# Kernel optimization log

Hardware: AMD Instinct MI355X
Metric: run time of the kernel (lower is better)

Reference implementation:

```python
import jax, jax.numpy as jnp
import numpy as np

B, H, W, C = 2, 96, 192, 768
NH, HD = 12, 64
W0, W1 = 8, 8          # window size
S0, S1 = 4, 4          # shift size
N = W0 * W1
NW = (H // W0) * (W // W1)
HID = 3072             # mlp_ratio 4 * dim
SCALE = HD ** -0.5


def _ln(x, g, b):
    m = x.mean(-1, keepdims=True)
    v = ((x - m) ** 2).mean(-1, keepdims=True)
    return (x - m) * jax.lax.rsqrt(v + 1e-5) * g + b


def _partition(x):  # (B,H,W,C) -> (B*NW, W0, W1, C)
    Bb = x.shape[0]
    x = x.reshape(Bb, H // W0, W0, W // W1, W1, -1).transpose(0, 1, 3, 2, 4, 5)
    return x.reshape(-1, W0, W1, x.shape[-1])


def _reverse(w):  # (B*NW, W0, W1, C) -> (B,H,W,C)
    Cc = w.shape[-1]
    x = w.reshape(B, H // W0, W // W1, W0, W1, Cc).transpose(0, 1, 3, 2, 4, 5)
    return x.reshape(B, H, W, Cc)


def _rope2(x):  # axial 2D RoPE on (nB, W0, W1, HD): first half rotates over h, second over w
    dh = HD // 2

    def cs(L, d):
        inv = 1.0 / (10000.0 ** (jnp.arange(0, d, 2, dtype=jnp.float32) / d))
        ang = jnp.arange(L, dtype=jnp.float32)[:, None] * inv
        return jnp.cos(ang), jnp.sin(ang)

    def rot(xa, cos, sin):
        x1, x2 = xa[..., 0::2], xa[..., 1::2]
        return jnp.stack([x1 * cos - x2 * sin, x1 * sin + x2 * cos], -1).reshape(xa.shape)

    ch, sh = cs(W0, dh)
    cw, sw = cs(W1, dh)
    xh = rot(x[..., :dh], ch[:, None, :], sh[:, None, :])
    xw = rot(x[..., dh:], cw[None, :, :], sw[None, :, :])
    return jnp.concatenate([xh, xw], -1)


def _make_mask():
    # faithful port of BasicLayer.create_mask (2D path)
    img = np.zeros((H, W), np.float32)
    cnt = 0
    for hs in (slice(0, -W0), slice(-W0, -S0), slice(-S0, None)):
        for wsl in (slice(0, -W1), slice(-W1, 0), slice(0, None)):
            img[hs, wsl] = cnt
            cnt += 1
    mw = img.reshape(H // W0, W0, W // W1, W1).transpose(0, 2, 1, 3).reshape(NW, N)
    am = mw[:, None, :] - mw[:, :, None]
    return jnp.asarray(np.where(am != 0, -100.0, 0.0).astype(np.float32))


def setup_inputs():
    key = jax.random.key(0)
    ks = jax.random.split(key, 6)
    s = lambda k, shape, fan: jax.random.normal(k, shape, jnp.float32) * (fan ** -0.5)
    return dict(
        x=jax.random.normal(ks[0], (B, H * W, C), jnp.float32),
        mask=_make_mask(),
        w_qkv=s(ks[1], (3 * C, C), C), b_qkv=jnp.zeros((3 * C,), jnp.float32),
        w_proj=s(ks[2], (C, C), C), b_proj=jnp.zeros((C,), jnp.float32),
        g1=jnp.ones((C,), jnp.float32), b1=jnp.zeros((C,), jnp.float32),
        g2=jnp.ones((C,), jnp.float32), b2=jnp.zeros((C,), jnp.float32),
        w_fc1=s(ks[3], (HID, C), C), b_fc1=jnp.zeros((HID,), jnp.float32),
        w_fc2=s(ks[4], (C, HID), HID), b_fc2=jnp.zeros((C,), jnp.float32),
    )


def reference(x, mask, w_qkv, b_qkv, w_proj, b_proj, g1, b1, g2, b2,
              w_fc1, b_fc1, w_fc2, b_fc2):
    shortcut = x
    xi = x.reshape(B, H, W, C)
    xi = jnp.roll(xi, (-S0, -S1), axis=(1, 2))
    xw = _partition(xi).reshape(-1, N, C)  # (B*NW, N, C)
    B_ = xw.shape[0]
    qkv = (xw @ w_qkv.T + b_qkv).reshape(B_, N, 3, NH, HD).transpose(2, 0, 3, 1, 4)
    q, k, v = qkv[0], qkv[1], qkv[2]  # (B_, NH, N, HD)
    q = _rope2(q.reshape(-1, W0, W1, HD)).reshape(B_, NH, N, HD)
    k = _rope2(k.reshape(-1, W0, W1, HD)).reshape(B_, NH, N, HD)
    attn = jnp.einsum('bhnd,bhmd->bhnm', q * SCALE, k)
    attn = attn.reshape(B, NW, NH, N, N) + mask[None, :, None]
    attn = jax.nn.softmax(attn.reshape(B_, NH, N, N), axis=-1)
    out = jnp.einsum('bhnm,bhmd->bnhd', attn, v).reshape(B_, N, C)
    out = out @ w_proj.T + b_proj
    xr = _reverse(out.reshape(-1, W0, W1, C))
    xr = jnp.roll(xr, (S0, S1), axis=(1, 2)).reshape(B, H * W, C)
    x1 = _ln(shortcut + xr, g1, b1)          # post-norm residual, as in source
    h = jax.nn.relu(x1 @ w_fc1.T + b_fc1) @ w_fc2.T + b_fc2
    return _ln(x1 + h, g2, b2)
```

## Files before the change

### kernel.cpp

```cpp
#include <hip/hip_runtime.h>
#include <math.h>
#include <stddef.h>

#define NTOK   36864
#define CDIM   768
#define HIDDIM 3072
#define QKVDIM 2304

typedef unsigned short u16;
typedef unsigned int   u32;
typedef __attribute__((ext_vector_type(8))) short short8;
typedef __attribute__((ext_vector_type(4))) float f32x4;

__device__ __forceinline__ float bf2f(u16 h) { return __uint_as_float(((u32)h) << 16); }
__device__ __forceinline__ u16 f2bf(float f) {
  u32 u = __float_as_uint(f);
  u32 r = u + 0x7fffu + ((u >> 16) & 1u);
  return (u16)(r >> 16);
}

__device__ __forceinline__ int win_row_to_src(int r) {
  int n = r & 63;
  int wflat = r >> 6;
  int b = wflat / 288;
  int wi = wflat - b * 288;
  int wh = wi / 24;
  int ww = wi - wh * 24;
  int i0 = n >> 3, i1 = n & 7;
  int hh = wh * 8 + i0 + 4; if (hh >= 96)  hh -= 96;
  int wp = ww * 8 + i1 + 4; if (wp >= 192) wp -= 192;
  return b * 18432 + hh * 192 + wp;
}

__device__ __forceinline__ void load_lds16(const u16* g, u16* l) {
  __builtin_amdgcn_global_load_lds((const __attribute__((address_space(1))) void*)g,
                                   (__attribute__((address_space(3))) void*)l, 16, 0, 0);
}

template<int OUTBF, int RELU, int RES>
__launch_bounds__(256)
__global__ void gemm_mfma(const u16* __restrict__ A, const u16* __restrict__ Wt,
                          const float* __restrict__ bias, const u16* __restrict__ res,
                          void* __restrict__ Cout, int M, int N, int K,
                          int gridx, int nwg)
{
  const int orig = blockIdx.x;
  const int xcd  = orig & 7;
  const int q    = nwg >> 3, r8 = nwg & 7;
  const int wgid = (xcd < r8 ? xcd * (q + 1) : r8 * (q + 1) + (xcd - r8) * q) + (orig >> 3);
  const int halfn = nwg >> 1, hc = gridx >> 1;
  const int half  = (wgid >= halfn) ? 1 : 0;
  const int w2    = wgid - half * halfn;
  const int bn    = (w2 % hc + half * hc) * 128;
  const int bm    = (w2 / hc) * 128;

  __shared__ u16 As[128 * 64];
  __shared__ u16 Bs[128 * 64];
  const int t    = threadIdx.x;
  const int wv   = t >> 6, lane = t & 63;
  const int wm   = wv >> 1, wn = wv & 1;
  const int lr   = lane & 15, lg = lane >> 4;
  const int srow = t >> 3;
  const int sslot= t & 7;

  const u16* Abase = A  + (size_t)bm * K;
  const u16* Bbase = Wt + (size_t)bn * K;

  f32x4 acc[4][4] = {};

  for (int k0 = 0; k0 < K; k0 += 64) {
#pragma unroll
    for (int i = 0; i < 4; i++) {
      int row  = i * 32 + srow;
      int slot = sslot ^ (row & 7);
      load_lds16(Abase + (size_t)row * K + k0 + slot * 8, As + t * 8 + i * 2048);
      load_lds16(Bbase + (size_t)row * K + k0 + slot * 8, Bs + t * 8 + i * 2048);
    }
    __syncthreads();

    short8 av[2][4], bv[2][4];
#pragma unroll
    for (int ks = 0; ks < 2; ks++) {
#pragma unroll
      for (int f = 0; f < 4; f++) {
        int ra = wm * 64 + f * 16 + lr;
        av[ks][f] = *(const short8*)(As + ra * 64 + (((ks * 4 + lg) ^ (ra & 7)) << 3));
        int rb = wn * 64 + f * 16 + lr;
        bv[ks][f] = *(const short8*)(Bs + rb * 64 + (((ks * 4 + lg) ^ (rb & 7)) << 3));
      }
    }
#pragma unroll
    for (int ks = 0; ks < 2; ks++)
#pragma unroll
      for (int mf = 0; mf < 4; mf++)
#pragma unroll
        for (int nf = 0; nf < 4; nf++)
          acc[mf][nf] = __builtin_amdgcn_mfma_f32_16x16x32_bf16(av[ks][mf], bv[ks][nf], acc[mf][nf], 0, 0, 0);
    __syncthreads();
  }

#pragma unroll
  for (int nf = 0; nf < 4; nf++) {
    int col = bn + wn * 64 + nf * 16 + lr;
    float bcol = bias[col];
#pragma unroll
    for (int mf = 0; mf < 4; mf++) {
#pragma unroll
      for (int j = 0; j < 4; j++) {
        int row = bm + wm * 64 + mf * 16 + lg * 4 + j;
        float v = acc[mf][nf][j] + bcol;
        if (RELU) v = fmaxf(v, 0.f);
        if (RES)  v += bf2f(res[(size_t)row * N + col]);
        if (OUTBF) ((u16*)Cout)[(size_t)row * N + col] = f2bf(v);
        else       ((float*)Cout)[(size_t)row * N + col] = v;
      }
    }
  }
}

__launch_bounds__(256)
__global__ void gather_x_bf16(const float* __restrict__ x, u16* __restrict__ xg)
{
  const int r = blockIdx.x, t = threadIdx.x;
  const float* src = x + (size_t)win_row_to_src(r) * CDIM;
  u16* dst = xg + (size_t)r * CDIM;
#pragma unroll
  for (int e = 0; e < 3; e++) dst[t + 256 * e] = f2bf(src[t + 256 * e]);
}

__launch_bounds__(256)
__global__ void conv_bf16(const float* __restrict__ in, u16* __restrict__ out, int n)
{
  int i = blockIdx.x * 256 + threadIdx.x;
  if (i < n) out[i] = f2bf(in[i]);
}

__launch_bounds__(256)
__global__ void attn_mfma(const u16* __restrict__ qkv, const float* __restrict__ mask,
                          u16* __restrict__ out, int bw0)
{
  __shared__ u16 vt[4][4096];
  __shared__ u16 pbuf[4][4096];
  __shared__ float ropetab[512];

  const int t = threadIdx.x;
  {
    int p = t >> 3, pos = t & 7;
    float inv = __expf(-(float)(p & 15) * 0.5756462732485115f);
    float sv, cv;
    sincosf((float)pos * inv, &sv, &cv);
    ropetab[t * 2]     = cv;
    ropetab[t * 2 + 1] = sv;
  }
  __syncthreads();

  const int wv = t >> 6, lane = t & 63;
  const int lr = lane & 15, lg = lane >> 4;
  const int gp   = blockIdx.x * 4 + wv;
  const int head = gp % 12;
  const int lw   = gp / 12;
  const int bwg  = bw0 + lw;
  const int widx = bwg % 288;
  const u16* base = qkv + (size_t)lw * 64 * QKVDIM + head * 64;

  {
    const u16* vrow = base + 1536 + (size_t)lane * QKVDIM;
    u16* vb = vt[wv];
#pragma unroll
    for (int s = 0; s < 8; s++) {
      short8 v = *(const short8*)(vrow + s * 8);
#pragma unroll
      for (int j = 0; j < 8; j++) {
        int d = s * 8 + j;
        vb[d * 64 + ((((lane >> 3) ^ (d & 7)) << 3) | (lane & 7))] = (u16)v[j];
      }
    }
  }

  short8 aq[4][2], ak[4][2];
#pragma unroll
  for (int f = 0; f < 4; f++) {
#pragma unroll
    for (int ks = 0; ks < 2; ks++) {
      int n = f * 16 + lr;
      short8 qv = *(const short8*)(base + (size_t)n * QKVDIM + ks * 32 + lg * 8);
      short8 kv = *(const short8*)(base + (size_t)n * QKVDIM + 768 + ks * 32 + lg * 8);
      short8 qo, ko;
#pragma unroll
      for (int jj = 0; jj < 4; jj++) {
        int p   = ks * 16 + lg * 4 + jj;
        int pos = (p < 16) ? (n >> 3) : (n & 7);
        float cv = ropetab[(p * 8 + pos) * 2];
        float sv = ropetab[(p * 8 + pos) * 2 + 1];
        float q1 = bf2f((u16)qv[2 * jj]), q2 = bf2f((u16)qv[2 * jj + 1]);
        float k1 = bf2f((u16)kv[2 * jj]), k2 = bf2f((u16)kv[2 * jj + 1]);
        qo[2 * jj]     = (short)f2bf((q1 * cv - q2 * sv) * 0.125f);
        qo[2 * jj + 1] = (short)f2bf((q1 * sv + q2 * cv) * 0.125f);
        ko[2 * jj]     = (short)f2bf(k1 * cv - k2 * sv);
        ko[2 * jj + 1] = (short)f2bf(k1 * sv + k2 * cv);
      }
      aq[f][ks] = qo; ak[f][ks] = ko;
    }
  }

  f32x4 sf[4][4] = {};
#pragma unroll
  for (int ks = 0; ks < 2; ks++)
#pragma unroll
    for (int fn = 0; fn < 4; fn++)
#pragma unroll
      for (int fm = 0; fm < 4; fm++)
        sf[fn][fm] = __builtin_amdgcn_mfma_f32_16x16x32_bf16(aq[fn][ks], ak[fm][ks], sf[fn][fm], 0, 0, 0);

  const float* mrow = mask + (size_t)widx * 4096;
#pragma unroll
  for (int fn = 0; fn < 4; fn++)
#pragma unroll
    for (int fm = 0; fm < 4; fm++)
#pragma unroll
      for (int j = 0; j < 4; j++)
        sf[fn][fm][j] += mrow[(fn * 16 + lg * 4 + j) * 64 + fm * 16 + lr];

#pragma unroll
  for (int fn = 0; fn < 4; fn++) {
#pragma unroll
    for (int j = 0; j < 4; j++) {
      float m0 = fmaxf(fmaxf(sf[fn][0][j], sf[fn][1][j]),
                       fmaxf(sf[fn][2][j], sf[fn][3][j]));
      m0 = fmaxf(m0, __shfl_xor(m0, 1));
      m0 = fmaxf(m0, __shfl_xor(m0, 2));
      m0 = fmaxf(m0, __shfl_xor(m0, 4));
      m0 = fmaxf(m0, __shfl_xor(m0, 8));
      float s0 = 0.f;
#pragma unroll
      for (int fm = 0; fm < 4; fm++) {
        float e = __expf(sf[fn][fm][j] - m0);
        sf[fn][fm][j] = e;
        s0 += e;
      }
      s0 += __shfl_xor(s0, 1);
      s0 += __shfl_xor(s0, 2);
      s0 += __shfl_xor(s0, 4);
      s0 += __shfl_xor(s0, 8);
      float r = 1.f / s0;
#pragma unroll
      for (int fm = 0; fm < 4; fm++) sf[fn][fm][j] *= r;
    }
  }

  u16* pb = pbuf[wv];
#pragma unroll
  for (int fn = 0; fn < 4; fn++)
#pragma unroll
    for (int fm = 0; fm < 4; fm++)
#pragma unroll
      for (int j = 0; j < 4; j++) {
        int n = fn * 16 + lg * 4 + j, m = fm * 16 + lr;
        pb[n * 64 + ((((m >> 3) ^ (n & 7)) << 3) | (m & 7))] = f2bf(sf[fn][fm][j]);
      }
  asm volatile("s_waitcnt lgkmcnt(0)" ::: "memory");

  short8 ap[4][2], bvf[4][2];
#pragma unroll
  for (int f = 0; f < 4; f++)
#pragma unroll
    for (int ks = 0; ks < 2; ks++) {
      int rn = f * 16 + lr;
      ap[f][ks]  = *(const short8*)(pb     + rn * 64 + (((ks * 4 + lg) ^ (rn & 7)) << 3));
      bvf[f][ks] = *(const short8*)(vt[wv] + rn * 64 + (((ks * 4 + lg) ^ (rn & 7)) << 3));
    }
  f32x4 o[4][4] = {};
#pragma unroll
  for (int ks = 0; ks < 2; ks++)
#pragma unroll
    for (int fn = 0; fn < 4; fn++)
#pragma unroll
      for (int fd = 0; fd < 4; fd++)
        o[fn][fd] = __builtin_amdgcn_mfma_f32_16x16x32_bf16(ap[fn][ks], bvf[fd][ks], o[fn][fd], 0, 0, 0);

  u16* ob = out + ((size_t)bwg * 64) * CDIM + head * 64;
#pragma unroll
  for (int fn = 0; fn < 4; fn++)
#pragma unroll
    for (int fd = 0; fd < 4; fd++)
#pragma unroll
      for (int j = 0; j < 4; j++) {
        int n = fn * 16 + lg * 4 + j, d = fd * 16 + lr;
        ob[(size_t)n * CDIM + d] = f2bf(o[fn][fd][j]);
      }
}

__launch_bounds__(256)
__global__ void ln1_kernel(const float* __restrict__ xin, const u16* __restrict__ add,
                           const float* __restrict__ g, const float* __restrict__ bb,
                           u16* __restrict__ out)
{
  const int tok = blockIdx.x;
  int b = tok / 18432;
  int hw = tok - b * 18432;
  int h = hw / 192, w = hw - h * 192;
  int h2 = h - 4; if (h2 < 0) h2 += 96;
  int w2 = w - 4; if (w2 < 0) w2 += 192;
  int r = ((b * 12 + (h2 >> 3)) * 24 + (w2 >> 3)) * 64 + (h2 & 7) * 8 + (w2 & 7);
  const float* a0 = xin + (size_t)tok * CDIM;
  const u16*   a1 = add + (size_t)r * CDIM;

  const int t = threadIdx.x;
  float v[3];
  float s1 = 0.f, s2 = 0.f;
#pragma unroll
  for (int e = 0; e < 3; e++) {
    float x = a0[t + 256 * e] + bf2f(a1[t + 256 * e]);
    v[e] = x; s1 += x; s2 += x * x;
  }
  __shared__ float r1[256], r2[256];
  r1[t] = s1; r2[t] = s2;
  __syncthreads();
  for (int o = 128; o > 0; o >>= 1) {
    if (t < o) { r1[t] += r1[t + o]; r2[t] += r2[t + o]; }
    __syncthreads();
  }
  float mean = r1[0] * (1.f / 768.f);
  float var  = r2[0] * (1.f / 768.f) - mean * mean;
  float rs   = rsqrtf(var + 1e-5f);
#pragma unroll
  for (int e = 0; e < 3; e++) {
    int c = t + 256 * e;
    out[(size_t)tok * CDIM + c] = f2bf((v[e] - mean) * rs * g[c] + bb[c]);
  }
}

__launch_bounds__(256)
__global__ void ln2_kernel(const u16* __restrict__ xin, const float* __restrict__ g,
                           const float* __restrict__ bb, float* __restrict__ out)
{
  const int tok = blockIdx.x;
  const u16* a0 = xin + (size_t)tok * CDIM;
  const int t = threadIdx.x;
  float v[3];
  float s1 = 0.f, s2 = 0.f;
#pragma unroll
  for (int e = 0; e < 3; e++) {
    float x = bf2f(a0[t + 256 * e]);
    v[e] = x; s1 += x; s2 += x * x;
  }
  __shared__ float r1[256], r2[256];
  r1[t] = s1; r2[t] = s2;
  __syncthreads();
  for (int o = 128; o > 0; o >>= 1) {
    if (t < o) { r1[t] += r1[t + o]; r2[t] += r2[t + o]; }
    __syncthreads();
  }
  float mean = r1[0] * (1.f / 768.f);
  float var  = r2[0] * (1.f / 768.f) - mean * mean;
  float rs   = rsqrtf(var + 1e-5f);
#pragma unroll
  for (int e = 0; e < 3; e++) {
    int c = t + 256 * e;
    out[(size_t)tok * CDIM + c] = (v[e] - mean) * rs * g[c] + bb[c];
  }
}

static inline void launch_gemm(const u16* A, const u16* Wt, const float* bias,
                               const u16* res, void* C, int M, int N, int K,
                               int outbf, int relu, int resf, hipStream_t s)
{
  int gridx = N / 128, nwg = gridx * (M / 128);
  if (outbf) {
    if (relu)      gemm_mfma<1,1,0><<<nwg, 256, 0, s>>>(A, Wt, bias, res, C, M, N, K, gridx, nwg);
    else if (resf) gemm_mfma<1,0,1><<<nwg, 256, 0, s>>>(A, Wt, bias, res, C, M, N, K, gridx, nwg);
    else           gemm_mfma<1,0,0><<<nwg, 256, 0, s>>>(A, Wt, bias, res, C, M, N, K, gridx, nwg);
  } else {
    gemm_mfma<0,0,0><<<nwg, 256, 0, s>>>(A, Wt, bias, res, C, M, N, K, gridx, nwg);
  }
}

extern "C" void kernel_launch(void* const* d_in, const int* in_sizes, int n_in,
                              void* d_out, int out_size, void* d_ws, size_t ws_size,
                              hipStream_t stream)
{
  const float* x      = (const float*)d_in[0];
  const float* mask   = (const float*)d_in[1];
  const float* w_qkv  = (const float*)d_in[2];
  const float* b_qkv  = (const float*)d_in[3];
  const float* w_proj = (const float*)d_in[4];
  const float* b_proj = (const float*)d_in[5];
  const float* g1     = (const float*)d_in[6];
  const float* b1     = (const float*)d_in[7];
  const float* g2     = (const float*)d_in[8];
  const float* b2     = (const float*)d_in[9];
  const float* w_fc1  = (const float*)d_in[10];
  const float* b_fc1  = (const float*)d_in[11];
  const float* w_fc2  = (const float*)d_in[12];
  const float* b_fc2  = (const float*)d_in[13];
  float* out = (float*)d_out;

  char* base = (char*)d_ws;
  u16* R1 = (u16*)base;
  u16* R2 = (u16*)(base + 56623104);
  u16* AO = R2 + 28311552;
  u16* R3 = (u16*)(base + 56623104 + 113246208);
  u16* wqkvb  = (u16*)(base + 56623104 + 113246208 + 56623104);
  u16* wprojb = wqkvb  + 1769472;
  u16* wfc1b  = wprojb + 589824;
  u16* wfc2b  = wfc1b  + 2359296;

  conv_bf16<<<(1769472 + 255) / 256, 256, 0, stream>>>(w_qkv,  wqkvb,  1769472);
  conv_bf16<<<( 589824 + 255) / 256, 256, 0, stream>>>(w_proj, wprojb,  589824);
  conv_bf16<<<(2359296 + 255) / 256, 256, 0, stream>>>(w_fc1,  wfc1b,  2359296);
  conv_bf16<<<(2359296 + 255) / 256, 256, 0, stream>>>(w_fc2,  wfc2b,  2359296);
  gather_x_bf16<<<NTOK, 256, 0, stream>>>(x, R1);

  for (int c = 0; c < 3; c++) {
    launch_gemm(R1 + (size_t)c * 12288 * CDIM, wqkvb, b_qkv, nullptr, R2,
                12288, QKVDIM, CDIM, 1, 0, 0, stream);
    attn_mfma<<<576, 256, 0, stream>>>(R2, mask, AO, c * 192);
  }

  launch_gemm(AO, wprojb, b_proj, nullptr, R3, NTOK, CDIM, CDIM, 1, 0, 0, stream);

  ln1_kernel<<<NTOK, 256, 0, stream>>>(x, R3, g1, b1, R1);

  for (int c = 0; c < 2; c++) {
    const u16* x1c = R1 + (size_t)c * 18432 * CDIM;
    launch_gemm(x1c, wfc1b, b_fc1, nullptr, R2, 18432, HIDDIM, CDIM, 1, 1, 0, stream);
    launch_gemm(R2, wfc2b, b_fc2, x1c, R3 + (size_t)c * 18432 * CDIM,
                18432, CDIM, HIDDIM, 1, 0, 1, stream);
  }

  ln2_kernel<<<NTOK, 256, 0, stream>>>(R3, g2, b2, out);
}
```

Before: 1.030 ms.

## Use 256x256 double-buffered GEMM tiles with 512 threads and split MFMA phases

Replaces the 128x128 single-buffered GEMM with a 256x256 tile kernel using 8 waves and a two-stage LDS double buffer. Global-to-LDS loads for tile k+2 are issued while MFMAs run on the current tile, with partial waitcnts and s_setprio to favour MFMA issue. The larger tile doubles operand reuse per LDS load. In exchange it uses 128KB of LDS per block, which limits occupancy, and leaves fewer workgroups to fill the CUs. It also adds a sched_barrier in the attention kernel.

```diff
diff --git a/kernel.cpp b/kernel.cpp
--- a/kernel.cpp
+++ b/kernel.cpp
@@ -38,65 +38,113 @@
 }
 
 template<int OUTBF, int RELU, int RES>
-__launch_bounds__(256)
-__global__ void gemm_mfma(const u16* __restrict__ A, const u16* __restrict__ Wt,
-                          const float* __restrict__ bias, const u16* __restrict__ res,
-                          void* __restrict__ Cout, int M, int N, int K,
-                          int gridx, int nwg)
+__launch_bounds__(512, 2)
+__global__ void gemm256(const u16* __restrict__ A, const u16* __restrict__ Wt,
+                        const float* __restrict__ bias, const u16* __restrict__ res,
+                        void* __restrict__ Cout, int M, int N, int K,
+                        int gridx, int nwg)
 {
   const int orig = blockIdx.x;
   const int xcd  = orig & 7;
   const int q    = nwg >> 3, r8 = nwg & 7;
   const int wgid = (xcd < r8 ? xcd * (q + 1) : r8 * (q + 1) + (xcd - r8) * q) + (orig >> 3);
-  const int halfn = nwg >> 1, hc = gridx >> 1;
-  const int half  = (wgid >= halfn) ? 1 : 0;
-  const int w2    = wgid - half * halfn;
-  const int bn    = (w2 % hc + half * hc) * 128;
-  const int bm    = (w2 / hc) * 128;
-
-  __shared__ u16 As[128 * 64];
-  __shared__ u16 Bs[128 * 64];
+  const int bn   = (wgid % gridx) * 256;
+  const int bm   = (wgid / gridx) * 256;
+
+  __shared__ __align__(16) u16 lds[2][2][256 * 64];
+
   const int t    = threadIdx.x;
   const int wv   = t >> 6, lane = t & 63;
-  const int wm   = wv >> 1, wn = wv & 1;
+  const int wm   = wv >> 2, wn = wv & 3;
   const int lr   = lane & 15, lg = lane >> 4;
-  const int srow = t >> 3;
-  const int sslot= t & 7;
+  const int sr   = t >> 3;
+  const int ss   = t & 7;
 
   const u16* Abase = A  + (size_t)bm * K;
   const u16* Bbase = Wt + (size_t)bn * K;
 
-  f32x4 acc[4][4] = {};
-
-  for (int k0 = 0; k0 < K; k0 += 64) {
-#pragma unroll
-    for (int i = 0; i < 4; i++) {
-      int row  = i * 32 + srow;
-      int slot = sslot ^ (row & 7);
-      load_lds16(Abase + (size_t)row * K + k0 + slot * 8, As + t * 8 + i * 2048);
-      load_lds16(Bbase + (size_t)row * K + k0 + slot * 8, Bs + t * 8 + i * 2048);
-    }
-    __syncthreads();
-
-    short8 av[2][4], bv[2][4];
-#pragma unroll
-    for (int ks = 0; ks < 2; ks++) {
-#pragma unroll
-      for (int f = 0; f < 4; f++) {
-        int ra = wm * 64 + f * 16 + lr;
-        av[ks][f] = *(const short8*)(As + ra * 64 + (((ks * 4 + lg) ^ (ra & 7)) << 3));
-        int rb = wn * 64 + f * 16 + lr;
-        bv[ks][f] = *(const short8*)(Bs + rb * 64 + (((ks * 4 + lg) ^ (rb & 7)) << 3));
-      }
-    }
+  const int nt = K >> 6;
+
+  auto stage = [&](int kt, int b) {
+    const int k0 = kt << 6;
+#pragma unroll
+    for (int j = 0; j < 4; j++) {
+      int row  = j * 64 + sr;
+      int slot = ss ^ (row & 7);
+      load_lds16(Abase + (size_t)row * K + k0 + slot * 8, &lds[b][0][j * 4096 + t * 8]);
+    }
+#pragma unroll
+    for (int j = 0; j < 4; j++) {
+      int row  = j * 64 + sr;
+      int slot = ss ^ (row & 7);
+      load_lds16(Bbase + (size_t)row * K + k0 + slot * 8, &lds[b][1][j * 4096 + t * 8]);
+    }
+  };
+
+  f32x4 acc[8][4] = {};
+
+  stage(0, 0);
+  stage(1, 1);
+
+  for (int tt = 0; tt < nt; tt++) {
+    const int cur = tt & 1;
+    if (tt + 1 < nt) asm volatile("s_waitcnt vmcnt(8)" ::: "memory");
+    else             asm volatile("s_waitcnt vmcnt(0)" ::: "memory");
+    __builtin_amdgcn_s_barrier();
+
+    const u16* Ab = &lds[cur][0][0];
+    const u16* Bb = &lds[cur][1][0];
+
+    short8 bfr[4][2], afr[4][2];
+#pragma unroll
+    for (int nf = 0; nf < 4; nf++)
+#pragma unroll
+      for (int ks = 0; ks < 2; ks++) {
+        int row = wn * 64 + nf * 16 + lr;
+        bfr[nf][ks] = *(const short8*)(Bb + row * 64 + (((ks * 4 + lg) ^ (row & 7)) << 3));
+      }
+#pragma unroll
+    for (int mf = 0; mf < 4; mf++)
+#pragma unroll
+      for (int ks = 0; ks < 2; ks++) {
+        int row = wm * 128 + mf * 16 + lr;
+        afr[mf][ks] = *(const short8*)(Ab + row * 64 + (((ks * 4 + lg) ^ (row & 7)) << 3));
+      }
+    asm volatile("s_waitcnt lgkmcnt(0)" ::: "memory");
+    __builtin_amdgcn_sched_barrier(0);
+    __builtin_amdgcn_s_setprio(1);
 #pragma unroll
     for (int ks = 0; ks < 2; ks++)
 #pragma unroll
       for (int mf = 0; mf < 4; mf++)
 #pragma unroll
         for (int nf = 0; nf < 4; nf++)
-          acc[mf][nf] = __builtin_amdgcn_mfma_f32_16x16x32_bf16(av[ks][mf], bv[ks][nf], acc[mf][nf], 0, 0, 0);
-    __syncthreads();
+          acc[mf][nf] = __builtin_amdgcn_mfma_f32_16x16x32_bf16(afr[mf][ks], bfr[nf][ks], acc[mf][nf], 0, 0, 0);
+    __builtin_amdgcn_s_setprio(0);
+
+    short8 afr2[4][2];
+#pragma unroll
+    for (int mf = 0; mf < 4; mf++)
+#pragma unroll
+      for (int ks = 0; ks < 2; ks++) {
+        int row = wm * 128 + (mf + 4) * 16 + lr;
+        afr2[mf][ks] = *(const short8*)(Ab + row * 64 + (((ks * 4 + lg) ^ (row & 7)) << 3));
+      }
+    asm volatile("s_waitcnt lgkmcnt(0)" ::: "memory");
+    __builtin_amdgcn_sched_barrier(0);
+    __builtin_amdgcn_s_barrier();
+
+    if (tt + 2 < nt) stage(tt + 2, cur);
+
+    __builtin_amdgcn_s_setprio(1);
+#pragma unroll
+    for (int ks = 0; ks < 2; ks++)
+#pragma unroll
+      for (int mf = 0; mf < 4; mf++)
+#pragma unroll
+        for (int nf = 0; nf < 4; nf++)
+          acc[mf + 4][nf] = __builtin_amdgcn_mfma_f32_16x16x32_bf16(afr2[mf][ks], bfr[nf][ks], acc[mf + 4][nf], 0, 0, 0);
+    __builtin_amdgcn_s_setprio(0);
   }
 
 #pragma unroll
@@ -104,10 +152,10 @@
     int col = bn + wn * 64 + nf * 16 + lr;
     float bcol = bias[col];
 #pragma unroll
-    for (int mf = 0; mf < 4; mf++) {
+    for (int mf = 0; mf < 8; mf++) {
 #pragma unroll
       for (int j = 0; j < 4; j++) {
-        int row = bm + wm * 64 + mf * 16 + lg * 4 + j;
+        int row = bm + wm * 128 + mf * 16 + lg * 4 + j;
         float v = acc[mf][nf][j] + bcol;
         if (RELU) v = fmaxf(v, 0.f);
         if (RES)  v += bf2f(res[(size_t)row * N + col]);
@@ -259,6 +307,7 @@
         pb[n * 64 + ((((m >> 3) ^ (n & 7)) << 3) | (m & 7))] = f2bf(sf[fn][fm][j]);
       }
   asm volatile("s_waitcnt lgkmcnt(0)" ::: "memory");
+  __builtin_amdgcn_sched_barrier(0);
 
   short8 ap[4][2], bvf[4][2];
 #pragma unroll
@@ -365,13 +414,13 @@
                                const u16* res, void* C, int M, int N, int K,
                                int outbf, int relu, int resf, hipStream_t s)
 {
-  int gridx = N / 128, nwg = gridx * (M / 128);
+  int gridx = N / 256, nwg = gridx * (M / 256);
   if (outbf) {
-    if (relu)      gemm_mfma<1,1,0><<<nwg, 256, 0, s>>>(A, Wt, bias, res, C, M, N, K, gridx, nwg);
-    else if (resf) gemm_mfma<1,0,1><<<nwg, 256, 0, s>>>(A, Wt, bias, res, C, M, N, K, gridx, nwg);
-    else           gemm_mfma<1,0,0><<<nwg, 256, 0, s>>>(A, Wt, bias, res, C, M, N, K, gridx, nwg);
+    if (relu)      gemm256<1,1,0><<<nwg, 512, 0, s>>>(A, Wt, bias, res, C, M, N, K, gridx, nwg);
+    else if (resf) gemm256<1,0,1><<<nwg, 512, 0, s>>>(A, Wt, bias, res, C, M, N, K, gridx, nwg);
+    else           gemm256<1,0,0><<<nwg, 512, 0, s>>>(A, Wt, bias, res, C, M, N, K, gridx, nwg);
   } else {
-    gemm_mfma<0,0,0><<<nwg, 256, 0, s>>>(A, Wt, bias, res, C, M, N, K, gridx, nwg);
+    gemm256<0,0,0><<<nwg, 512, 0, s>>>(A, Wt, bias, res, C, M, N, K, gridx, nwg);
   }
 }
 
```

Result: faster. 953.8 us (-7.4%).
